# Optimization experiments

Hardware: AMD Instinct MI355X
Metric: run time of the kernel (lower is better)

Reference implementation:

```python
import jax, jax.numpy as jnp
import numpy as np

NUM_TOPICS = 100
VOCAB = 8192
MC_N = 20
MD_N = 20
LAMBDA_D = 0.7
LAMBDA_A = 100.0
WARMUP_RATIO = 0.5
NUM_EPOCHS = 200


def setup_inputs() -> dict:
    key = jax.random.key(0)
    k1, k2 = jax.random.split(key)
    beta = jax.random.normal(k1, (NUM_TOPICS, VOCAB), dtype=jnp.float32)
    W = jax.random.uniform(k2, (VOCAB, VOCAB), dtype=jnp.float32)
    # fill_diagonal_(1) in __init__
    d = jnp.arange(VOCAB)
    W = W.at[d, d].set(1.0)
    return {"beta": beta, "coherence_weight": W, "epoch": 120}


def reference(beta, coherence_weight, epoch):
    K, V = beta.shape
    rows = jnp.arange(K)[:, None]

    # --- Mc: top-Mc_n mask -> additive -99999 on non-topk entries ---
    _, mc_idx = jax.lax.top_k(beta, MC_N)                      # [K, Mc_n]
    Mc = jnp.zeros_like(beta).at[rows, mc_idx].set(1.0)        # [K, V]
    Mc_add = (1.0 - Mc) * (-99999.0)

    # softmax over masked beta is detached in the original
    p = jax.lax.stop_gradient(jax.nn.softmax(beta + Mc_add, axis=1))
    M = p @ coherence_weight                                    # [K, V]

    # row-wise min-max normalize, then Wc = 1 - normalized
    m_min = jnp.min(M, axis=1, keepdims=True)
    m_max = jnp.max(M, axis=1, keepdims=True)
    Wc = 1.0 - (M - m_min) / (m_max - m_min)

    loss = 100.0 * jax.nn.softmax(beta, axis=1) ** 2 * Wc       # [K, V]

    # --- diversity mask Md (lambda_d > 0.5 branch) ---
    _, md_idx = jax.lax.top_k(beta, MD_N)
    Md_mask = jnp.zeros_like(beta).at[rows, md_idx].set(1.0)    # [K, V]
    # Md[t, v] = any other row has v in its top-Md_n
    col_sum = jnp.sum(Md_mask, axis=0)                          # [V]
    Md = (col_sum[None, :] - Md_mask) > 0                       # [K, V] bool

    pos = jnp.sum(jnp.where(Md, loss, 0.0))
    neg = jnp.sum(jnp.where(Md, 0.0, loss))
    total = (pos * LAMBDA_D + neg * (1.0 - LAMBDA_D)) * 2.0

    warmup_epochs = int(WARMUP_RATIO * NUM_EPOCHS)              # 100
    lambda_a_delta = LAMBDA_A / warmup_epochs
    lambda_a = epoch * lambda_a_delta if epoch < warmup_epochs else LAMBDA_A
    return lambda_a * total
```

## Files before the change

kernel.cpp:

```cpp
#include <hip/hip_runtime.h>
#include <math.h>

#define NT 100
#define VOCAB 8192
#define TOPN 20
#define NWV 4
#define WCOLS 2048
#define SCAP 256
#define CHUNKS 8
#define CCOLS 1024
#define NB (NT * CHUNKS)

__global__ __launch_bounds__(256) void topk_kernel(
    const float* __restrict__ beta,
    int*   __restrict__ top_idx,
    float* __restrict__ top_p,
    float* __restrict__ rowstats)
{
    const int k = blockIdx.x;
    const int t = threadIdx.x;
    const int wv = t >> 6;
    const int lane = t & 63;

    __shared__ float cu[NWV * SCAP];
    __shared__ int   cid[NWV * SCAP];
    __shared__ float smaxs[NWV], ssums[NWV];
    __shared__ float pv[NWV * TOPN];
    __shared__ int   pid[NWV * TOPN];
    __shared__ float s_winv[TOPN];
    __shared__ int   s_wini[TOPN];
    __shared__ float s_ps, s_rowmax;

    const float* base = beta + (size_t)k * VOCAB + wv * WCOLS;
    float4 r[8];
    float mx = -INFINITY;
#pragma unroll
    for (int i = 0; i < 8; ++i) {
        r[i] = *reinterpret_cast<const float4*>(base + (size_t)(i * 64 + lane) * 4);
        mx = fmaxf(mx, fmaxf(fmaxf(r[i].x, r[i].y), fmaxf(r[i].z, r[i].w)));
    }
#pragma unroll
    for (int off = 32; off >= 1; off >>= 1) mx = fmaxf(mx, __shfl_xor(mx, off));
    const float smax = mx;

    float se = 0.f;
#pragma unroll
    for (int i = 0; i < 8; ++i) {
        se += expf(r[i].x - smax) + expf(r[i].y - smax)
            + expf(r[i].z - smax) + expf(r[i].w - smax);
    }
#pragma unroll
    for (int off = 32; off >= 1; off >>= 1) se += __shfl_xor(se, off);
    const float ssum = se;

    if (lane == 0) { smaxs[wv] = smax; ssums[wv] = ssum; }

    float T = smax - 1.5f;
    for (int g = 0; g < 16; ++g) {
        int c = 0;
#pragma unroll
        for (int i = 0; i < 8; ++i) {
            c += (r[i].x >= T) + (r[i].y >= T) + (r[i].z >= T) + (r[i].w >= T);
        }
#pragma unroll
        for (int off = 32; off >= 1; off >>= 1) c += __shfl_xor(c, off);
        if (c >= TOPN) break;
        T -= 0.4f;
    }

    int wbase = 0;
#pragma unroll
    for (int i = 0; i < 8; ++i) {
#pragma unroll
        for (int e = 0; e < 4; ++e) {
            const float v = (&r[i].x)[e];
            const bool pr = (v >= T);
            const unsigned long long mask = __ballot(pr);
            const int pre = __popcll(mask & ((1ull << lane) - 1ull));
            if (pr) {
                const int p = wbase + pre;
                if (p < SCAP) {
                    cu[wv * SCAP + p]  = v;
                    cid[wv * SCAP + p] = wv * WCOLS + (i * 64 + lane) * 4 + e;
                }
            }
            wbase += __popcll(mask);
        }
    }
    const int n = min(wbase, SCAP);

    for (int it = 0; it < TOPN; ++it) {
        float bv = -INFINITY; int bp = -1;
        for (int p = lane; p < n; p += 64) {
            const float v = cu[wv * SCAP + p];
            if (v > bv) { bv = v; bp = p; }
        }
#pragma unroll
        for (int off = 32; off >= 1; off >>= 1) {
            const float ov = __shfl_down(bv, off);
            const int   op = __shfl_down(bp, off);
            if (ov > bv) { bv = ov; bp = op; }
        }
        bp = __shfl(bp, 0);
        bv = __shfl(bv, 0);
        if (lane == 0) {
            pv[wv * TOPN + it]  = bv;
            pid[wv * TOPN + it] = (bp >= 0) ? cid[wv * SCAP + bp] : 0;
        }
        if (bp >= 0) cu[wv * SCAP + bp] = -INFINITY;
    }
    __syncthreads();

    if (wv == 0) {
        for (int it = 0; it < TOPN; ++it) {
            float bv = -INFINITY; int bp = -1;
            for (int p = lane; p < NWV * TOPN; p += 64) {
                const float v = pv[p];
                if (v > bv) { bv = v; bp = p; }
            }
#pragma unroll
            for (int off = 32; off >= 1; off >>= 1) {
                const float ov = __shfl_down(bv, off);
                const int   op = __shfl_down(bp, off);
                if (ov > bv) { bv = ov; bp = op; }
            }
            bp = __shfl(bp, 0);
            bv = __shfl(bv, 0);
            if (lane == 0) { s_winv[it] = bv; s_wini[it] = pid[bp]; }
            pv[bp] = -INFINITY;
        }
        if (lane == 0) {
            const float rowmax = s_winv[0];
            float ps = 0.f;
#pragma unroll
            for (int j = 0; j < TOPN; ++j) ps += expf(s_winv[j] - rowmax);
            float rs = 0.f;
#pragma unroll
            for (int s = 0; s < NWV; ++s) rs += ssums[s] * expf(smaxs[s] - rowmax);
            s_rowmax = rowmax;
            s_ps = ps;
            rowstats[2 * k + 0] = rowmax;
            rowstats[2 * k + 1] = rs;
        }
    }
    __syncthreads();
    if (t < TOPN) {
        top_idx[k * TOPN + t] = s_wini[t];
        top_p[k * TOPN + t]   = expf(s_winv[t] - s_rowmax) / s_ps;
    }
}

__global__ __launch_bounds__(256) void fused_kernel(
    const float* __restrict__ beta,
    const float* __restrict__ W,
    const int*   __restrict__ top_idx,
    const float* __restrict__ top_p,
    const float* __restrict__ rowstats,
    float* __restrict__ part6)
{
    const int b = blockIdx.x;
    const int k = b / CHUNKS;
    const int c = b % CHUNKS;
    const int t = threadIdx.x;

    __shared__ int   sIdx[TOPN];
    __shared__ float sP[TOPN];
    __shared__ int   cnt[CCOLS];
    __shared__ float sA[4], sB[4], sC[4], sD[4], sE[4], sF[4];

    if (t < TOPN) { sIdx[t] = top_idx[k * TOPN + t]; sP[t] = top_p[k * TOPN + t]; }
#pragma unroll
    for (int i = 0; i < CCOLS / 256; ++i) cnt[i * 256 + t] = 0;
    __syncthreads();

    int   idx_r[TOPN];
    float p_r[TOPN];
#pragma unroll
    for (int j = 0; j < TOPN; ++j) { idx_r[j] = sIdx[j]; p_r[j] = sP[j]; }

    const int lo  = c * CCOLS;
    const int col = lo + t * 4;
    float4 w_r[TOPN];
#pragma unroll
    for (int j = 0; j < TOPN; ++j)
        w_r[j] = *reinterpret_cast<const float4*>(W + (size_t)idx_r[j] * VOCAB + col);
    const float4 bv = *reinterpret_cast<const float4*>(beta + (size_t)k * VOCAB + col);

#pragma unroll 8
    for (int e = t; e < NT * TOPN; e += 256) {
        const int v = top_idx[e] - lo;
        if ((unsigned)v < (unsigned)CCOLS) atomicAdd(&cnt[v], 1);
    }
    __syncthreads();
    if (t < TOPN) {
        const int v = sIdx[t] - lo;
        if ((unsigned)v < (unsigned)CCOLS) atomicSub(&cnt[v], 1);
    }

    float4 m = make_float4(0.f, 0.f, 0.f, 0.f);
#pragma unroll
    for (int j = 0; j < TOPN; ++j) {
        const float pj = p_r[j];
        m.x += pj * w_r[j].x; m.y += pj * w_r[j].y;
        m.z += pj * w_r[j].z; m.w += pj * w_r[j].w;
    }

    float mn  = fminf(fminf(m.x, m.y), fminf(m.z, m.w));
    float mxv = fmaxf(fmaxf(m.x, m.y), fmaxf(m.z, m.w));

    const float rmax = rowstats[2 * k + 0];
    const float rinv = 1.0f / rowstats[2 * k + 1];
    float4 w4;
    w4.x = expf(bv.x - rmax) * rinv;  w4.x = 100.f * w4.x * w4.x;
    w4.y = expf(bv.y - rmax) * rinv;  w4.y = 100.f * w4.y * w4.y;
    w4.z = expf(bv.z - rmax) * rinv;  w4.z = 100.f * w4.z * w4.z;
    w4.w = expf(bv.w - rmax) * rinv;  w4.w = 100.f * w4.w * w4.w;

    __syncthreads();

    float Apos = 0.f, Bpos = 0.f, Aneg = 0.f, Bneg = 0.f;
    {
        const int lc = t * 4;
        if (cnt[lc + 0] > 0) { Apos += w4.x; Bpos += w4.x * m.x; } else { Aneg += w4.x; Bneg += w4.x * m.x; }
        if (cnt[lc + 1] > 0) { Apos += w4.y; Bpos += w4.y * m.y; } else { Aneg += w4.y; Bneg += w4.y * m.y; }
        if (cnt[lc + 2] > 0) { Apos += w4.z; Bpos += w4.z * m.z; } else { Aneg += w4.z; Bneg += w4.z * m.z; }
        if (cnt[lc + 3] > 0) { Apos += w4.w; Bpos += w4.w * m.w; } else { Aneg += w4.w; Bneg += w4.w * m.w; }
    }

#pragma unroll
    for (int off = 32; off >= 1; off >>= 1) {
        mn   = fminf(mn,  __shfl_down(mn,  off));
        mxv  = fmaxf(mxv, __shfl_down(mxv, off));
        Apos += __shfl_down(Apos, off);
        Bpos += __shfl_down(Bpos, off);
        Aneg += __shfl_down(Aneg, off);
        Bneg += __shfl_down(Bneg, off);
    }
    if ((t & 63) == 0) {
        const int w = t >> 6;
        sA[w] = mn; sB[w] = mxv; sC[w] = Apos; sD[w] = Bpos; sE[w] = Aneg; sF[w] = Bneg;
    }
    __syncthreads();
    if (t == 0) {
        part6[b * 6 + 0] = fminf(fminf(sA[0], sA[1]), fminf(sA[2], sA[3]));
        part6[b * 6 + 1] = fmaxf(fmaxf(sB[0], sB[1]), fmaxf(sB[2], sB[3]));
        part6[b * 6 + 2] = sC[0] + sC[1] + sC[2] + sC[3];
        part6[b * 6 + 3] = sD[0] + sD[1] + sD[2] + sD[3];
        part6[b * 6 + 4] = sE[0] + sE[1] + sE[2] + sE[3];
        part6[b * 6 + 5] = sF[0] + sF[1] + sF[2] + sF[3];
    }
}

__global__ __launch_bounds__(128) void finalize_kernel(
    const float* __restrict__ part6,
    const int*   __restrict__ epoch,
    float* __restrict__ out)
{
    const int t = threadIdx.x;
    __shared__ float sp[128], sn[128];
    float pos = 0.f, neg = 0.f;
    if (t < NT) {
        float mn = INFINITY, mxv = -INFINITY;
        float Ap = 0.f, Bp = 0.f, An = 0.f, Bn = 0.f;
        for (int cc = 0; cc < CHUNKS; ++cc) {
            const float* p6 = part6 + (size_t)(t * CHUNKS + cc) * 6;
            mn  = fminf(mn,  p6[0]);
            mxv = fmaxf(mxv, p6[1]);
            Ap += p6[2]; Bp += p6[3]; An += p6[4]; Bn += p6[5];
        }
        const float inv = 1.0f / (mxv - mn);
        pos = Ap - inv * (Bp - mn * Ap);
        neg = An - inv * (Bn - mn * An);
    }
    sp[t] = pos; sn[t] = neg;
    __syncthreads();
    if (t == 0) {
        float P = 0.f, N = 0.f;
        for (int i = 0; i < NT; ++i) { P += sp[i]; N += sn[i]; }
        const float total = (P * 0.7f + N * 0.3f) * 2.0f;
        const int e = *epoch;
        const float la = (e < 100) ? (float)e : 100.0f;
        *out = la * total;
    }
}

extern "C" void kernel_launch(void* const* d_in, const int* in_sizes, int n_in,
                              void* d_out, int out_size, void* d_ws, size_t ws_size,
                              hipStream_t stream)
{
    (void)in_sizes; (void)n_in; (void)out_size; (void)ws_size;
    const float* beta  = (const float*)d_in[0];
    const float* W     = (const float*)d_in[1];
    const int*   epoch = (const int*)d_in[2];
    float* out = (float*)d_out;

    char* ws = (char*)d_ws;
    int*   top_idx  = (int*)ws;    ws += NT * TOPN * sizeof(int);
    float* top_p    = (float*)ws;  ws += NT * TOPN * sizeof(float);
    float* rowstats = (float*)ws;  ws += NT * 2 * sizeof(float);
    float* part6    = (float*)ws;  ws += NB * 6 * sizeof(float);

    topk_kernel<<<NT, 256, 0, stream>>>(beta, top_idx, top_p, rowstats);
    fused_kernel<<<NB, 256, 0, stream>>>(beta, W, top_idx, top_p, rowstats, part6);
    finalize_kernel<<<1, 128, 0, stream>>>(part6, epoch, out);
}
```

Baseline: 47.09 us.

## Merge finalize into fused kernel with one 1024-thread block per topic row

```diff
diff --git a/kernel.cpp b/kernel.cpp
--- a/kernel.cpp
+++ b/kernel.cpp
@@ -7,20 +7,19 @@
 #define NWV 4
 #define WCOLS 2048
 #define SCAP 256
-#define CHUNKS 8
-#define CCOLS 1024
-#define NB (NT * CHUNKS)
 
 __global__ __launch_bounds__(256) void topk_kernel(
     const float* __restrict__ beta,
     int*   __restrict__ top_idx,
     float* __restrict__ top_p,
-    float* __restrict__ rowstats)
+    float* __restrict__ rowstats,
+    float* __restrict__ out)
 {
     const int k = blockIdx.x;
     const int t = threadIdx.x;
     const int wv = t >> 6;
     const int lane = t & 63;
+    if (k == 0 && t == 0) *out = 0.f;
 
     __shared__ float cu[NWV * SCAP];
     __shared__ int   cid[NWV * SCAP];
@@ -150,81 +149,71 @@
     }
 }
 
-__global__ __launch_bounds__(256) void fused_kernel(
+__global__ __launch_bounds__(1024) void fused_kernel(
     const float* __restrict__ beta,
     const float* __restrict__ W,
     const int*   __restrict__ top_idx,
     const float* __restrict__ top_p,
     const float* __restrict__ rowstats,
-    float* __restrict__ part6)
+    const int*   __restrict__ epoch,
+    float* __restrict__ out)
 {
-    const int b = blockIdx.x;
-    const int k = b / CHUNKS;
-    const int c = b % CHUNKS;
+    const int k = blockIdx.x;
     const int t = threadIdx.x;
 
+    __shared__ int   cnt[VOCAB];
     __shared__ int   sIdx[TOPN];
     __shared__ float sP[TOPN];
-    __shared__ int   cnt[CCOLS];
-    __shared__ float sA[4], sB[4], sC[4], sD[4], sE[4], sF[4];
+    __shared__ float sA[16], sB[16], sC[16], sD[16], sE[16], sF[16];
 
     if (t < TOPN) { sIdx[t] = top_idx[k * TOPN + t]; sP[t] = top_p[k * TOPN + t]; }
 #pragma unroll
-    for (int i = 0; i < CCOLS / 256; ++i) cnt[i * 256 + t] = 0;
-    __syncthreads();
+    for (int i = 0; i < VOCAB / 1024; ++i) cnt[i * 1024 + t] = 0;
+    __syncthreads();
+
+#pragma unroll 2
+    for (int e = t; e < NT * TOPN; e += 1024) atomicAdd(&cnt[top_idx[e]], 1);
+    if (t < TOPN) atomicSub(&cnt[sIdx[t]], 1);
 
     int   idx_r[TOPN];
     float p_r[TOPN];
 #pragma unroll
     for (int j = 0; j < TOPN; ++j) { idx_r[j] = sIdx[j]; p_r[j] = sP[j]; }
 
-    const int lo  = c * CCOLS;
-    const int col = lo + t * 4;
-    float4 w_r[TOPN];
-#pragma unroll
-    for (int j = 0; j < TOPN; ++j)
-        w_r[j] = *reinterpret_cast<const float4*>(W + (size_t)idx_r[j] * VOCAB + col);
-    const float4 bv = *reinterpret_cast<const float4*>(beta + (size_t)k * VOCAB + col);
-
-#pragma unroll 8
-    for (int e = t; e < NT * TOPN; e += 256) {
-        const int v = top_idx[e] - lo;
-        if ((unsigned)v < (unsigned)CCOLS) atomicAdd(&cnt[v], 1);
-    }
-    __syncthreads();
-    if (t < TOPN) {
-        const int v = sIdx[t] - lo;
-        if ((unsigned)v < (unsigned)CCOLS) atomicSub(&cnt[v], 1);
-    }
-
-    float4 m = make_float4(0.f, 0.f, 0.f, 0.f);
-#pragma unroll
-    for (int j = 0; j < TOPN; ++j) {
-        const float pj = p_r[j];
-        m.x += pj * w_r[j].x; m.y += pj * w_r[j].y;
-        m.z += pj * w_r[j].z; m.w += pj * w_r[j].w;
-    }
-
-    float mn  = fminf(fminf(m.x, m.y), fminf(m.z, m.w));
-    float mxv = fmaxf(fmaxf(m.x, m.y), fmaxf(m.z, m.w));
-
     const float rmax = rowstats[2 * k + 0];
     const float rinv = 1.0f / rowstats[2 * k + 1];
-    float4 w4;
-    w4.x = expf(bv.x - rmax) * rinv;  w4.x = 100.f * w4.x * w4.x;
-    w4.y = expf(bv.y - rmax) * rinv;  w4.y = 100.f * w4.y * w4.y;
-    w4.z = expf(bv.z - rmax) * rinv;  w4.z = 100.f * w4.z * w4.z;
-    w4.w = expf(bv.w - rmax) * rinv;  w4.w = 100.f * w4.w * w4.w;
-
-    __syncthreads();
-
+
+    __syncthreads();
+
+    float mn = INFINITY, mxv = -INFINITY;
     float Apos = 0.f, Bpos = 0.f, Aneg = 0.f, Bneg = 0.f;
-    {
-        const int lc = t * 4;
-        if (cnt[lc + 0] > 0) { Apos += w4.x; Bpos += w4.x * m.x; } else { Aneg += w4.x; Bneg += w4.x * m.x; }
-        if (cnt[lc + 1] > 0) { Apos += w4.y; Bpos += w4.y * m.y; } else { Aneg += w4.y; Bneg += w4.y * m.y; }
-        if (cnt[lc + 2] > 0) { Apos += w4.z; Bpos += w4.z * m.z; } else { Aneg += w4.z; Bneg += w4.z * m.z; }
-        if (cnt[lc + 3] > 0) { Apos += w4.w; Bpos += w4.w * m.w; } else { Aneg += w4.w; Bneg += w4.w * m.w; }
+
+#pragma unroll
+    for (int seg = 0; seg < 2; ++seg) {
+        const int col = seg * 4096 + t * 4;
+
+        float4 m = make_float4(0.f, 0.f, 0.f, 0.f);
+#pragma unroll
+        for (int j = 0; j < TOPN; ++j) {
+            const float4 w = *reinterpret_cast<const float4*>(W + (size_t)idx_r[j] * VOCAB + col);
+            const float pj = p_r[j];
+            m.x += pj * w.x; m.y += pj * w.y; m.z += pj * w.z; m.w += pj * w.w;
+        }
+        mn  = fminf(mn,  fminf(fminf(m.x, m.y), fminf(m.z, m.w)));
+        mxv = fmaxf(mxv, fmaxf(fmaxf(m.x, m.y), fmaxf(m.z, m.w)));
+
+        const float4 bv = *reinterpret_cast<const float4*>(beta + (size_t)k * VOCAB + col);
+        float4 w4;
+        w4.x = expf(bv.x - rmax) * rinv;  w4.x = 100.f * w4.x * w4.x;
+        w4.y = expf(bv.y - rmax) * rinv;  w4.y = 100.f * w4.y * w4.y;
+        w4.z = expf(bv.z - rmax) * rinv;  w4.z = 100.f * w4.z * w4.z;
+        w4.w = expf(bv.w - rmax) * rinv;  w4.w = 100.f * w4.w * w4.w;
+
+        const int4 c4 = *reinterpret_cast<const int4*>(cnt + col);
+        if (c4.x > 0) { Apos += w4.x; Bpos += w4.x * m.x; } else { Aneg += w4.x; Bneg += w4.x * m.x; }
+        if (c4.y > 0) { Apos += w4.y; Bpos += w4.y * m.y; } else { Aneg += w4.y; Bneg += w4.y * m.y; }
+        if (c4.z > 0) { Apos += w4.z; Bpos += w4.z * m.z; } else { Aneg += w4.z; Bneg += w4.z * m.z; }
+        if (c4.w > 0) { Apos += w4.w; Bpos += w4.w * m.w; } else { Aneg += w4.w; Bneg += w4.w * m.w; }
     }
 
 #pragma unroll
@@ -242,45 +231,19 @@
     }
     __syncthreads();
     if (t == 0) {
-        part6[b * 6 + 0] = fminf(fminf(sA[0], sA[1]), fminf(sA[2], sA[3]));
-        part6[b * 6 + 1] = fmaxf(fmaxf(sB[0], sB[1]), fmaxf(sB[2], sB[3]));
-        part6[b * 6 + 2] = sC[0] + sC[1] + sC[2] + sC[3];
-        part6[b * 6 + 3] = sD[0] + sD[1] + sD[2] + sD[3];
-        part6[b * 6 + 4] = sE[0] + sE[1] + sE[2] + sE[3];
-        part6[b * 6 + 5] = sF[0] + sF[1] + sF[2] + sF[3];
-    }
-}
-
-__global__ __launch_bounds__(128) void finalize_kernel(
-    const float* __restrict__ part6,
-    const int*   __restrict__ epoch,
-    float* __restrict__ out)
-{
-    const int t = threadIdx.x;
-    __shared__ float sp[128], sn[128];
-    float pos = 0.f, neg = 0.f;
-    if (t < NT) {
-        float mn = INFINITY, mxv = -INFINITY;
-        float Ap = 0.f, Bp = 0.f, An = 0.f, Bn = 0.f;
-        for (int cc = 0; cc < CHUNKS; ++cc) {
-            const float* p6 = part6 + (size_t)(t * CHUNKS + cc) * 6;
-            mn  = fminf(mn,  p6[0]);
-            mxv = fmaxf(mxv, p6[1]);
-            Ap += p6[2]; Bp += p6[3]; An += p6[4]; Bn += p6[5];
-        }
-        const float inv = 1.0f / (mxv - mn);
-        pos = Ap - inv * (Bp - mn * Ap);
-        neg = An - inv * (Bn - mn * An);
-    }
-    sp[t] = pos; sn[t] = neg;
-    __syncthreads();
-    if (t == 0) {
-        float P = 0.f, N = 0.f;
-        for (int i = 0; i < NT; ++i) { P += sp[i]; N += sn[i]; }
-        const float total = (P * 0.7f + N * 0.3f) * 2.0f;
+        float a = sA[0], b = sB[0], Ap = 0.f, Bp = 0.f, An = 0.f, Bn = 0.f;
+#pragma unroll
+        for (int w = 0; w < 16; ++w) {
+            a  = fminf(a, sA[w]);
+            b  = fmaxf(b, sB[w]);
+            Ap += sC[w]; Bp += sD[w]; An += sE[w]; Bn += sF[w];
+        }
+        const float inv = 1.0f / (b - a);
+        const float pos = Ap - inv * (Bp - a * Ap);
+        const float neg = An - inv * (Bn - a * An);
         const int e = *epoch;
         const float la = (e < 100) ? (float)e : 100.0f;
-        *out = la * total;
+        atomicAdd(out, la * (pos * 0.7f + neg * 0.3f) * 2.0f);
     }
 }
 
@@ -298,9 +261,7 @@
     int*   top_idx  = (int*)ws;    ws += NT * TOPN * sizeof(int);
     float* top_p    = (float*)ws;  ws += NT * TOPN * sizeof(float);
     float* rowstats = (float*)ws;  ws += NT * 2 * sizeof(float);
-    float* part6    = (float*)ws;  ws += NB * 6 * sizeof(float);
-
-    topk_kernel<<<NT, 256, 0, stream>>>(beta, top_idx, top_p, rowstats);
-    fused_kernel<<<NB, 256, 0, stream>>>(beta, W, top_idx, top_p, rowstats, part6);
-    finalize_kernel<<<1, 128, 0, stream>>>(part6, epoch, out);
+
+    topk_kernel<<<NT, 256, 0, stream>>>(beta, top_idx, top_p, rowstats, out);
+    fused_kernel<<<NT, 1024, 0, stream>>>(beta, W, top_idx, top_p, rowstats, epoch, out);
 }
```

Result: no change. 46.47 us, median of 2 (-1.3%).
